# Optimization experiments

Hardware: AMD Instinct MI355X
Metric: run time of the kernel (lower is better)

## Reference

```python
import jax, jax.numpy as jnp
import numpy as np

E = 512
H = 8
D = E // H
WIN = 128  # mask_window_size


def setup_inputs() -> dict:
    key = jax.random.key(0)
    k1, k2, k3, k4, k5 = jax.random.split(key, 5)
    B, L = 2, 4096
    s = 1.0 / np.sqrt(E)
    return {
        "x": jax.random.normal(k1, (B, L, E), dtype=jnp.float32),
        "in_proj_w": jax.random.normal(k2, (3 * E, E), dtype=jnp.float32) * s,
        "in_proj_b": jax.random.normal(k3, (3 * E,), dtype=jnp.float32) * 0.02,
        "out_w": jax.random.normal(k4, (E, E), dtype=jnp.float32) * s,
        "out_b": jax.random.normal(k5, (E,), dtype=jnp.float32) * 0.02,
    }


def reference(x, in_proj_w, in_proj_b, out_w, out_b):
    B, L, _ = x.shape
    # fused qkv projection (torch MultiheadAttention in_proj): x @ W.T + b
    qkv = jnp.einsum("ble,fe->blf", x, in_proj_w) + in_proj_b  # [B,L,3E]
    q, k, v = jnp.split(qkv, 3, axis=-1)
    # [B,H,L,D]
    q = q.reshape(B, L, H, D).transpose(0, 2, 1, 3)
    k = k.reshape(B, L, H, D).transpose(0, 2, 1, 3)
    v = v.reshape(B, L, H, D).transpose(0, 2, 1, 3)
    scores = jnp.einsum("bhqd,bhkd->bhqk", q, k) / jnp.sqrt(jnp.float32(D))
    # (diagonal stays blocked — faithful to the original gen_mask quirk)
    idx = jnp.arange(L)
    dist = jnp.abs(idx[:, None] - idx[None, :])
    blocked = (dist > WIN) | (dist == 0)  # [L,L]
    scores = jnp.where(blocked[None, None], -jnp.inf, scores)
    attn = jax.nn.softmax(scores, axis=-1)  # [B,H,L,L]
    out = jnp.einsum("bhqk,bhkd->bhqd", attn, v)  # [B,H,L,D]
    out = out.transpose(0, 2, 1, 3).reshape(B, L, E)
    return jnp.einsum("ble,fe->blf", out, out_w) + out_b
```

## Files before the change

### kernel.cpp

```cpp
#include <hip/hip_runtime.h>
#include <math.h>

#define E_DIM 512
#define H_DIM 8
#define WIN 128
#define L_SEQ 4096
#define B_SZ 2

typedef unsigned short ushort_t;
typedef unsigned int uint_t;
typedef __attribute__((ext_vector_type(8))) __bf16 bf16x8;
typedef __attribute__((ext_vector_type(4))) float f32x4;

__device__ __forceinline__ ushort_t f2bf(float f) {
    uint_t u = __float_as_uint(f);
    u = u + 0x7fffu + ((u >> 16) & 1u);
    return (ushort_t)(u >> 16);
}
__device__ __forceinline__ float bf2f(ushort_t h) {
    return __uint_as_float((uint_t)h << 16);
}

__device__ __forceinline__ void gload16(const ushort_t* g, ushort_t* l) {
    __builtin_amdgcn_global_load_lds(
        (const __attribute__((address_space(1))) void*)g,
        (__attribute__((address_space(3))) void*)l,
        16, 0, 0);
}


__global__ __launch_bounds__(256) void convertX(
    const float* __restrict__ x,  ushort_t* __restrict__ xh,
    const float* __restrict__ w1, ushort_t* __restrict__ w1h,
    const float* __restrict__ w2, ushort_t* __restrict__ w2h) {
    int sg = blockIdx.x * 256 + threadIdx.x;
    const float* src; ushort_t* dh;
    if (sg < 524288)      { src = x;  dh = xh; }
    else if (sg < 622592) { src = w1; dh = w1h; sg -= 524288; }
    else                  { src = w2; dh = w2h; sg -= 622592; }
    const int tile = sg >> 6, slot = sg & 63;
    const int row = (tile >> 4) * 16 + (slot & 15);
    const int k   = (tile & 15) * 32 + (slot >> 4) * 8;
    const float4 v0 = *(const float4*)&src[(size_t)row * 512 + k];
    const float4 v1 = *(const float4*)&src[(size_t)row * 512 + k + 4];
    const float vv[8] = {v0.x, v0.y, v0.z, v0.w, v1.x, v1.y, v1.z, v1.w};
    union { ushort_t u[8]; ushort4 v[2]; } h;
    #pragma unroll
    for (int j = 0; j < 8; j++) h.u[j] = f2bf(vv[j]);
    ((ushort4*)(dh + (size_t)sg * 8))[0] = h.v[0];
    ((ushort4*)(dh + (size_t)sg * 8))[1] = h.v[1];
}

__global__ __launch_bounds__(256) void gemm_qkv(
    const ushort_t* __restrict__ Ah,
    const ushort_t* __restrict__ Wh,
    const float* __restrict__ bias,
    ushort_t* __restrict__ qTh, ushort_t* __restrict__ qTl,
    ushort_t* __restrict__ kTh, ushort_t* __restrict__ kTl,
    ushort_t* __restrict__ vTh) {
    __shared__ __align__(16) ushort_t sAh[2][8 * 512];
    __shared__ __align__(16) ushort_t sWh[2][8 * 512];

    const int tid = threadIdx.x, lane = tid & 63, w = tid >> 6;
    const int wm = w & 1, wn = w >> 1, ln = lane & 15, quad = lane >> 4;
    const int bx = blockIdx.x, by = blockIdx.y;
    const int lo8 = lane * 8;
    const int wu = __builtin_amdgcn_readfirstlane(w);

    f32x4 acc[4][4];
    const f32x4 zero = {0.f, 0.f, 0.f, 0.f};
    #pragma unroll
    for (int i = 0; i < 4; i++)
        #pragma unroll
        for (int j = 0; j < 4; j++) acc[i][j] = zero;

    const ushort_t* pb[4];
    ushort_t* db0[4];
    ushort_t* db1[4];
    #pragma unroll
    for (int t = 0; t < 4; t++) {
        const int g = wu * 4 + t;
        if (g < 8) {
            pb[t] = Ah + ((size_t)(bx * 8 + g) * 16) * 512;
            db0[t] = &sAh[0][g * 512]; db1[t] = &sAh[1][g * 512];
        } else {
            const int u = g - 8;
            pb[t] = Wh + ((size_t)(by * 8 + u) * 16) * 512;
            db0[t] = &sWh[0][u * 512]; db1[t] = &sWh[1][u * 512];
        }
    }

    #pragma unroll
    for (int t = 0; t < 4; t++)
        gload16(pb[t] + lo8, db0[t]);

    for (int kt = 0; kt < 16; kt++) {
        __syncthreads();
        if (kt < 15) {
            const int koff = (kt + 1) * 512;
            if ((kt + 1) & 1) {
                #pragma unroll
                for (int t = 0; t < 4; t++) gload16(pb[t] + koff + lo8, db1[t]);
            } else {
                #pragma unroll
                for (int t = 0; t < 4; t++) gload16(pb[t] + koff + lo8, db0[t]);
            }
        }
        const int cb = kt & 1;
        bf16x8 fah[4];
        #pragma unroll
        for (int i = 0; i < 4; i++)
            fah[i] = *(const bf16x8*)&sAh[cb][(wm * 4 + i) * 512 + lo8];
        #pragma unroll
        for (int j = 0; j < 4; j++) {
            const bf16x8 fbh = *(const bf16x8*)&sWh[cb][(wn * 4 + j) * 512 + lo8];
            #pragma unroll
            for (int i = 0; i < 4; i++)
                acc[i][j] = __builtin_amdgcn_mfma_f32_16x16x32_bf16(fah[i], fbh, acc[i][j], 0, 0, 0);
        }
    }

    const int b = bx >> 5;
    const int h = 2 * (by & 3) + wn;
    if (by < 8) {
        ushort_t* dh = (by < 4) ? qTh : kTh;
        ushort_t* dl = (by < 4) ? qTl : kTl;
        #pragma unroll
        for (int i = 0; i < 4; i++) {
            const int rt = (bx & 31) * 8 + wm * 4 + i;
            const size_t tb = ((size_t)(b * 8 + h) * 256 + rt) * 2;
            #pragma unroll
            for (int j = 0; j < 4; j++) {
                const float bv = bias[by * 128 + wn * 64 + j * 16 + ln];
                const size_t tile = tb + (j >> 1);
                #pragma unroll
                for (int r = 0; r < 4; r++) {
                    const int slot = ((j * 2 + (ln >> 3)) & 3) * 16 + quad * 4 + r;
                    const size_t idx = tile * 512 + slot * 8 + (ln & 7);
                    const float v = acc[i][j][r] + bv;
                    const ushort_t hh = f2bf(v);
                    dh[idx] = hh;
                    dl[idx] = f2bf(v - bf2f(hh));
                }
            }
        }
    } else {
        const int kwin = (bx & 31) * 2 + wm;
        #pragma unroll
        for (int i = 0; i < 4; i++) {
            const int kk = i >> 1;
            #pragma unroll
            for (int j = 0; j < 4; j++) {
                const float bv = bias[by * 128 + wn * 64 + j * 16 + ln];
                const size_t tile = (((size_t)(b * 8 + h) * 64 + kwin) * 4 + j) * 2 + kk;
                #pragma unroll
                for (int r = 0; r < 4; r++) {
                    const int klq = quad * 4 + r;
                    const int slot = ((i & 1) * 2 + (klq >> 3)) * 16 + ln;
                    const size_t idx = tile * 512 + slot * 8 + (klq & 7);
                    vTh[idx] = f2bf(acc[i][j][r] + bv);
                }
            }
        }
    }
}

__global__ __launch_bounds__(512) void attn_mfma(
    const ushort_t* __restrict__ qTh, const ushort_t* __restrict__ qTl,
    const ushort_t* __restrict__ kTh, const ushort_t* __restrict__ kTl,
    const ushort_t* __restrict__ vTh,
    ushort_t* __restrict__ outh) {
    __shared__ __align__(16) ushort_t sKh[8 * 512];
    __shared__ __align__(16) ushort_t sKl[8 * 512];
    __shared__ __align__(16) ushort_t sV [8 * 512];
    __shared__ __align__(16) ushort_t sP [16 * 512];

    const int qs = blockIdx.x * 128;
    const int h = blockIdx.y, b = blockIdx.z;
    const int bh = b * 8 + h;
    const int tid = threadIdx.x, lane = tid & 63;
    const int w = tid >> 6, ln = lane & 15, quad = lane >> 4;
    const int lo8 = lane * 8;

    bf16x8 qf[2][2];
    {
        const size_t qt = ((size_t)bh * 256 + (qs >> 4) + w) * 2;
        qf[0][0] = *(const bf16x8*)(qTh + (qt + 0) * 512 + lo8);
        qf[1][0] = *(const bf16x8*)(qTh + (qt + 1) * 512 + lo8);
        qf[0][1] = *(const bf16x8*)(qTl + (qt + 0) * 512 + lo8);
        qf[1][1] = *(const bf16x8*)(qTl + (qt + 1) * 512 + lo8);
    }

    f32x4 oacc[4];
    const f32x4 zero = {0.f, 0.f, 0.f, 0.f};
    #pragma unroll
    for (int dt = 0; dt < 4; dt++) oacc[dt] = zero;
    float m_run[4], l_run[4];
    #pragma unroll
    for (int r = 0; r < 4; r++) { m_run[r] = -1e30f; l_run[r] = 0.f; }

    const float cscale = 0.125f * 1.44269504f;
    const int qlo = qs + 16 * w;

    for (int kt = 0; kt < 6; kt++) {
        const int ks = qs - 128 + kt * 64;

        __syncthreads();

        if (w < 4) {
            int st = (qs >> 4) - 8 + kt * 4 + w;
            st = st < 0 ? 0 : (st > 255 ? 255 : st);
            const size_t kb = ((size_t)bh * 256 + st) * 2 * 512 + lo8;
            gload16(kTh + kb,       &sKh[(w * 2 + 0) * 512]);
            gload16(kTh + kb + 512, &sKh[(w * 2 + 1) * 512]);
            gload16(kTl + kb,       &sKl[(w * 2 + 0) * 512]);
            gload16(kTl + kb + 512, &sKl[(w * 2 + 1) * 512]);
        } else {
            const int u = w - 4;
            int vw = (qs >> 6) - 2 + kt;
            vw = vw < 0 ? 0 : (vw > 63 ? 63 : vw);
            const size_t vb = (((size_t)bh * 64 + vw) * 4 + u) * 2 * 512 + lo8;
            gload16(vTh + vb,       &sV[(u * 2 + 0) * 512]);
            gload16(vTh + vb + 512, &sV[(u * 2 + 1) * 512]);
        }
        __syncthreads();

        f32x4 sacc[4];
        #pragma unroll
        for (int jt = 0; jt < 4; jt++) {
            f32x4 a = zero;
            const int klo = ks + 16 * jt;
            const bool dead = (klo > qlo + 15 + WIN) || (klo + 15 < qlo - WIN) ||
                              (klo >= L_SEQ) || (klo + 15 < 0);
            if (!dead) {
                #pragma unroll
                for (int kk = 0; kk < 2; kk++) {
                    const bf16x8 kh = *(const bf16x8*)&sKh[(jt * 2 + kk) * 512 + lo8];
                    const bf16x8 klo2 = *(const bf16x8*)&sKl[(jt * 2 + kk) * 512 + lo8];
                    a = __builtin_amdgcn_mfma_f32_16x16x32_bf16(qf[kk][0], kh, a, 0, 0, 0);
                    a = __builtin_amdgcn_mfma_f32_16x16x32_bf16(qf[kk][0], klo2, a, 0, 0, 0);
                    a = __builtin_amdgcn_mfma_f32_16x16x32_bf16(qf[kk][1], kh, a, 0, 0, 0);
                }
            }
            sacc[jt] = a;
        }

        float u[4][4];
        #pragma unroll
        for (int jt = 0; jt < 4; jt++) {
            const int kcol = ks + 16 * jt + ln;
            #pragma unroll
            for (int r = 0; r < 4; r++) {
                const int qrow = qlo + quad * 4 + r;
                const int dist = qrow > kcol ? qrow - kcol : kcol - qrow;
                const bool ok = (kcol >= 0) && (kcol < L_SEQ) && (dist >= 1) && (dist <= WIN);
                u[jt][r] = ok ? sacc[jt][r] * cscale : -INFINITY;
            }
        }
        float mk[4];
        #pragma unroll
        for (int r = 0; r < 4; r++)
            mk[r] = fmaxf(fmaxf(u[0][r], u[1][r]), fmaxf(u[2][r], u[3][r]));
        #pragma unroll
        for (int off = 1; off <= 8; off <<= 1)
            #pragma unroll
            for (int r = 0; r < 4; r++)
                mk[r] = fmaxf(mk[r], __shfl_xor(mk[r], off));

        float alpha[4], psum[4], p[4][4];
        #pragma unroll
        for (int r = 0; r < 4; r++) {
            const float mnew = fmaxf(fmaxf(m_run[r], mk[r]), -1e30f);
            alpha[r] = exp2f(m_run[r] - mnew);
            m_run[r] = mnew;
            psum[r] = 0.f;
            #pragma unroll
            for (int jt = 0; jt < 4; jt++) {
                p[jt][r] = exp2f(u[jt][r] - mnew);
                psum[r] += p[jt][r];
            }
        }
        #pragma unroll
        for (int off = 1; off <= 8; off <<= 1)
            #pragma unroll
            for (int r = 0; r < 4; r++)
                psum[r] += __shfl_xor(psum[r], off);
        #pragma unroll
        for (int r = 0; r < 4; r++)
            l_run[r] = l_run[r] * alpha[r] + psum[r];

        #pragma unroll
        for (int dt = 0; dt < 4; dt++)
            #pragma unroll
            for (int r = 0; r < 4; r++)
                oacc[dt][r] *= alpha[r];

        #pragma unroll
        for (int jt = 0; jt < 4; jt++)
            #pragma unroll
            for (int r = 0; r < 4; r++) {
                const int slot = ((jt & 1) * 2 + (ln >> 3)) * 16 + quad * 4 + r;
                sP[w * 1024 + (jt >> 1) * 512 + slot * 8 + (ln & 7)] = f2bf(p[jt][r]);
            }

        #pragma unroll
        for (int kk = 0; kk < 2; kk++) {
            const bf16x8 pf = *(const bf16x8*)&sP[w * 1024 + kk * 512 + lo8];
            #pragma unroll
            for (int dt = 0; dt < 4; dt++) {
                const bf16x8 vf = *(const bf16x8*)&sV[(dt * 2 + kk) * 512 + lo8];
                oacc[dt] = __builtin_amdgcn_mfma_f32_16x16x32_bf16(pf, vf, oacc[dt], 0, 0, 0);
            }
        }
    }

    const int Rt = ((b * L_SEQ + qs) >> 4) + w;
    #pragma unroll
    for (int r = 0; r < 4; r++) {
        const float inv_l = 1.f / l_run[r];
        #pragma unroll
        for (int dt = 0; dt < 4; dt++) {
            const float v = oacc[dt][r] * inv_l;
            const int tile = Rt * 16 + h * 2 + (dt >> 1);
            const int slot = ((dt & 1) * 2 + (ln >> 3)) * 16 + quad * 4 + r;
            const size_t idx = (size_t)tile * 512 + slot * 8 + (ln & 7);
            outh[idx] = f2bf(v);
        }
    }
}

__global__ __launch_bounds__(512) void gemm_out(
    const ushort_t* __restrict__ Ah,
    const ushort_t* __restrict__ Wh,
    const float* __restrict__ bias, float* __restrict__ C) {
    __shared__ __align__(16) ushort_t sAh[2][16 * 512];
    __shared__ __align__(16) ushort_t sWh[2][8 * 512];

    const int tid = threadIdx.x, lane = tid & 63, w = tid >> 6;
    const int wm = w & 3, wn = w >> 2, ln = lane & 15, quad = lane >> 4;
    const int bx = blockIdx.x, by = blockIdx.y;
    const int lo8 = lane * 8;
    const int wu = __builtin_amdgcn_readfirstlane(w);

    f32x4 acc[2][2];
    const f32x4 zero = {0.f, 0.f, 0.f, 0.f};
    #pragma unroll
    for (int i = 0; i < 2; i++)
        #pragma unroll
        for (int j = 0; j < 2; j++) acc[i][j] = zero;

    const ushort_t* pb[3];
    ushort_t* db0[3];
    ushort_t* db1[3];
    #pragma unroll
    for (int t = 0; t < 3; t++) {
        const int g = wu * 3 + t;
        if (g < 16) {
            pb[t] = Ah + ((size_t)(bx * 8 + (g >> 1)) * 16 + (g & 1)) * 512;
            db0[t] = &sAh[0][g * 512]; db1[t] = &sAh[1][g * 512];
        } else {
            const int u = g - 16;
            pb[t] = Wh + ((size_t)(by * 4 + (u >> 1)) * 16 + (u & 1)) * 512;
            db0[t] = &sWh[0][u * 512]; db1[t] = &sWh[1][u * 512];
        }
    }

    #pragma unroll
    for (int t = 0; t < 3; t++)
        gload16(pb[t] + lo8, db0[t]);

    for (int KT = 0; KT < 8; KT++) {
        __syncthreads();
        if (KT < 7) {
            const int koff = (KT + 1) * 1024;
            if ((KT + 1) & 1) {
                #pragma unroll
                for (int t = 0; t < 3; t++) gload16(pb[t] + koff + lo8, db1[t]);
            } else {
                #pragma unroll
                for (int t = 0; t < 3; t++) gload16(pb[t] + koff + lo8, db0[t]);
            }
        }
        const int cb = KT & 1;
        #pragma unroll
        for (int ks = 0; ks < 2; ks++) {
            bf16x8 fah[2];
            #pragma unroll
            for (int i = 0; i < 2; i++)
                fah[i] = *(const bf16x8*)&sAh[cb][((wm * 2 + i) * 2 + ks) * 512 + lo8];
            #pragma unroll
            for (int j = 0; j < 2; j++) {
                const bf16x8 fbh = *(const bf16x8*)&sWh[cb][((wn * 2 + j) * 2 + ks) * 512 + lo8];
                #pragma unroll
                for (int i = 0; i < 2; i++)
                    acc[i][j] = __builtin_amdgcn_mfma_f32_16x16x32_bf16(fah[i], fbh, acc[i][j], 0, 0, 0);
            }
        }
    }

    #pragma unroll
    for (int i = 0; i < 2; i++) {
        const int row0 = bx * 128 + wm * 32 + i * 16 + quad * 4;
        #pragma unroll
        for (int j = 0; j < 2; j++) {
            const int col = by * 64 + wn * 32 + j * 16 + ln;
            const float bv = bias[col];
            #pragma unroll
            for (int r = 0; r < 4; r++)
                C[(size_t)(row0 + r) * E_DIM + col] = acc[i][j][r] + bv;
        }
    }
}

extern "C" void kernel_launch(void* const* d_in, const int* in_sizes, int n_in,
                              void* d_out, int out_size, void* d_ws, size_t ws_size,
                              hipStream_t stream) {
    const float* x         = (const float*)d_in[0];
    const float* in_proj_w = (const float*)d_in[1];
    const float* in_proj_b = (const float*)d_in[2];
    const float* out_w     = (const float*)d_in[3];
    const float* out_b     = (const float*)d_in[4];
    float* out = (float*)d_out;

    const int N = B_SZ * L_SEQ;
    const size_t NE = (size_t)N * E_DIM;

    char* p = (char*)d_ws;
    ushort_t* xh  = (ushort_t*)p; p += NE * 2;
    ushort_t* w1h = (ushort_t*)p; p += (size_t)3 * E_DIM * E_DIM * 2;
    ushort_t* w2h = (ushort_t*)p; p += (size_t)E_DIM * E_DIM * 2;
    ushort_t* qTh = (ushort_t*)p; p += NE * 2;
    ushort_t* qTl = (ushort_t*)p; p += NE * 2;
    ushort_t* kTh = (ushort_t*)p; p += NE * 2;
    ushort_t* kTl = (ushort_t*)p; p += NE * 2;
    ushort_t* vTh = (ushort_t*)p; p += NE * 2;
    ushort_t* ath = (ushort_t*)p; p += NE * 2;

    convertX<<<2560, 256, 0, stream>>>(x, xh, in_proj_w, w1h, out_w, w2h);

    gemm_qkv<<<dim3(64, 12), 256, 0, stream>>>(
        xh, w1h, in_proj_b, qTh, qTl, kTh, kTl, vTh);

    attn_mfma<<<dim3(L_SEQ / 128, H_DIM, B_SZ), 512, 0, stream>>>(
        qTh, qTl, kTh, kTl, vTh, ath);

    gemm_out<<<dim3(64, 8), 512, 0, stream>>>(
        ath, w2h, out_b, out);
}
```

Baseline: 144.3 us.

## Drop bf16 hi/lo split for Q and K and double-buffer K/V tiles

Q and K are now stored as a single bf16 copy instead of a high/low pair. This halves QKV-projection stores and attention loads, and cuts the QK^T MFMAs from three per step to one. The freed shared memory double-buffers the K and V tiles, so the next tile's loads are issued before the current tile's compute and the second barrier per iteration is gone. In exchange, attention scores lose the extra precision the split gave, so accuracy may drift against an fp32 reference.

```diff
diff --git a/kernel.cpp b/kernel.cpp
--- a/kernel.cpp
+++ b/kernel.cpp
@@ -55,8 +55,8 @@
     const ushort_t* __restrict__ Ah,
     const ushort_t* __restrict__ Wh,
     const float* __restrict__ bias,
-    ushort_t* __restrict__ qTh, ushort_t* __restrict__ qTl,
-    ushort_t* __restrict__ kTh, ushort_t* __restrict__ kTl,
+    ushort_t* __restrict__ qTh,
+    ushort_t* __restrict__ kTh,
     ushort_t* __restrict__ vTh) {
     __shared__ __align__(16) ushort_t sAh[2][8 * 512];
     __shared__ __align__(16) ushort_t sWh[2][8 * 512];
@@ -124,7 +124,6 @@
     const int h = 2 * (by & 3) + wn;
     if (by < 8) {
         ushort_t* dh = (by < 4) ? qTh : kTh;
-        ushort_t* dl = (by < 4) ? qTl : kTl;
         #pragma unroll
         for (int i = 0; i < 4; i++) {
             const int rt = (bx & 31) * 8 + wm * 4 + i;
@@ -137,10 +136,7 @@
                 for (int r = 0; r < 4; r++) {
                     const int slot = ((j * 2 + (ln >> 3)) & 3) * 16 + quad * 4 + r;
                     const size_t idx = tile * 512 + slot * 8 + (ln & 7);
-                    const float v = acc[i][j][r] + bv;
-                    const ushort_t hh = f2bf(v);
-                    dh[idx] = hh;
-                    dl[idx] = f2bf(v - bf2f(hh));
+                    dh[idx] = f2bf(acc[i][j][r] + bv);
                 }
             }
         }
@@ -166,13 +162,12 @@
 }
 
 __global__ __launch_bounds__(512) void attn_mfma(
-    const ushort_t* __restrict__ qTh, const ushort_t* __restrict__ qTl,
-    const ushort_t* __restrict__ kTh, const ushort_t* __restrict__ kTl,
+    const ushort_t* __restrict__ qTh,
+    const ushort_t* __restrict__ kTh,
     const ushort_t* __restrict__ vTh,
     ushort_t* __restrict__ outh) {
-    __shared__ __align__(16) ushort_t sKh[8 * 512];
-    __shared__ __align__(16) ushort_t sKl[8 * 512];
-    __shared__ __align__(16) ushort_t sV [8 * 512];
+    __shared__ __align__(16) ushort_t sKh[2][8 * 512];
+    __shared__ __align__(16) ushort_t sV [2][8 * 512];
     __shared__ __align__(16) ushort_t sP [16 * 512];
 
     const int qs = blockIdx.x * 128;
@@ -182,13 +177,11 @@
     const int w = tid >> 6, ln = lane & 15, quad = lane >> 4;
     const int lo8 = lane * 8;
 
-    bf16x8 qf[2][2];
+    bf16x8 qf[2];
     {
         const size_t qt = ((size_t)bh * 256 + (qs >> 4) + w) * 2;
-        qf[0][0] = *(const bf16x8*)(qTh + (qt + 0) * 512 + lo8);
-        qf[1][0] = *(const bf16x8*)(qTh + (qt + 1) * 512 + lo8);
-        qf[0][1] = *(const bf16x8*)(qTl + (qt + 0) * 512 + lo8);
-        qf[1][1] = *(const bf16x8*)(qTl + (qt + 1) * 512 + lo8);
+        qf[0] = *(const bf16x8*)(qTh + (qt + 0) * 512 + lo8);
+        qf[1] = *(const bf16x8*)(qTh + (qt + 1) * 512 + lo8);
     }
 
     f32x4 oacc[4];
@@ -202,28 +195,46 @@
     const float cscale = 0.125f * 1.44269504f;
     const int qlo = qs + 16 * w;
 
+    {
+        if (w < 4) {
+            int st = (qs >> 4) - 8 + w;
+            st = st < 0 ? 0 : (st > 255 ? 255 : st);
+            const size_t kb = ((size_t)bh * 256 + st) * 2 * 512 + lo8;
+            gload16(kTh + kb,       &sKh[0][(w * 2 + 0) * 512]);
+            gload16(kTh + kb + 512, &sKh[0][(w * 2 + 1) * 512]);
+        } else {
+            const int u = w - 4;
+            int vw = (qs >> 6) - 2;
+            vw = vw < 0 ? 0 : (vw > 63 ? 63 : vw);
+            const size_t vb = (((size_t)bh * 64 + vw) * 4 + u) * 2 * 512 + lo8;
+            gload16(vTh + vb,       &sV[0][(u * 2 + 0) * 512]);
+            gload16(vTh + vb + 512, &sV[0][(u * 2 + 1) * 512]);
+        }
+    }
+
     for (int kt = 0; kt < 6; kt++) {
         const int ks = qs - 128 + kt * 64;
 
         __syncthreads();
 
-        if (w < 4) {
-            int st = (qs >> 4) - 8 + kt * 4 + w;
-            st = st < 0 ? 0 : (st > 255 ? 255 : st);
-            const size_t kb = ((size_t)bh * 256 + st) * 2 * 512 + lo8;
-            gload16(kTh + kb,       &sKh[(w * 2 + 0) * 512]);
-            gload16(kTh + kb + 512, &sKh[(w * 2 + 1) * 512]);
-            gload16(kTl + kb,       &sKl[(w * 2 + 0) * 512]);
-            gload16(kTl + kb + 512, &sKl[(w * 2 + 1) * 512]);
-        } else {
-            const int u = w - 4;
-            int vw = (qs >> 6) - 2 + kt;
-            vw = vw < 0 ? 0 : (vw > 63 ? 63 : vw);
-            const size_t vb = (((size_t)bh * 64 + vw) * 4 + u) * 2 * 512 + lo8;
-            gload16(vTh + vb,       &sV[(u * 2 + 0) * 512]);
-            gload16(vTh + vb + 512, &sV[(u * 2 + 1) * 512]);
-        }
-        __syncthreads();
+        if (kt < 5) {
+            const int nb = (kt + 1) & 1;
+            if (w < 4) {
+                int st = (qs >> 4) - 8 + (kt + 1) * 4 + w;
+                st = st < 0 ? 0 : (st > 255 ? 255 : st);
+                const size_t kb = ((size_t)bh * 256 + st) * 2 * 512 + lo8;
+                gload16(kTh + kb,       &sKh[nb][(w * 2 + 0) * 512]);
+                gload16(kTh + kb + 512, &sKh[nb][(w * 2 + 1) * 512]);
+            } else {
+                const int u = w - 4;
+                int vw = (qs >> 6) - 2 + kt + 1;
+                vw = vw < 0 ? 0 : (vw > 63 ? 63 : vw);
+                const size_t vb = (((size_t)bh * 64 + vw) * 4 + u) * 2 * 512 + lo8;
+                gload16(vTh + vb,       &sV[nb][(u * 2 + 0) * 512]);
+                gload16(vTh + vb + 512, &sV[nb][(u * 2 + 1) * 512]);
+            }
+        }
+        const int cb = kt & 1;
 
         f32x4 sacc[4];
         #pragma unroll
@@ -235,11 +246,8 @@
             if (!dead) {
                 #pragma unroll
                 for (int kk = 0; kk < 2; kk++) {
-                    const bf16x8 kh = *(const bf16x8*)&sKh[(jt * 2 + kk) * 512 + lo8];
-                    const bf16x8 klo2 = *(const bf16x8*)&sKl[(jt * 2 + kk) * 512 + lo8];
-                    a = __builtin_amdgcn_mfma_f32_16x16x32_bf16(qf[kk][0], kh, a, 0, 0, 0);
-                    a = __builtin_amdgcn_mfma_f32_16x16x32_bf16(qf[kk][0], klo2, a, 0, 0, 0);
-                    a = __builtin_amdgcn_mfma_f32_16x16x32_bf16(qf[kk][1], kh, a, 0, 0, 0);
+                    const bf16x8 kh = *(const bf16x8*)&sKh[cb][(jt * 2 + kk) * 512 + lo8];
+                    a = __builtin_amdgcn_mfma_f32_16x16x32_bf16(qf[kk], kh, a, 0, 0, 0);
                 }
             }
             sacc[jt] = a;
@@ -308,7 +316,7 @@
             const bf16x8 pf = *(const bf16x8*)&sP[w * 1024 + kk * 512 + lo8];
             #pragma unroll
             for (int dt = 0; dt < 4; dt++) {
-                const bf16x8 vf = *(const bf16x8*)&sV[(dt * 2 + kk) * 512 + lo8];
+                const bf16x8 vf = *(const bf16x8*)&sV[cb][(dt * 2 + kk) * 512 + lo8];
                 oacc[dt] = __builtin_amdgcn_mfma_f32_16x16x32_bf16(pf, vf, oacc[dt], 0, 0, 0);
             }
         }
@@ -430,19 +438,17 @@
     ushort_t* w1h = (ushort_t*)p; p += (size_t)3 * E_DIM * E_DIM * 2;
     ushort_t* w2h = (ushort_t*)p; p += (size_t)E_DIM * E_DIM * 2;
     ushort_t* qTh = (ushort_t*)p; p += NE * 2;
-    ushort_t* qTl = (ushort_t*)p; p += NE * 2;
     ushort_t* kTh = (ushort_t*)p; p += NE * 2;
-    ushort_t* kTl = (ushort_t*)p; p += NE * 2;
     ushort_t* vTh = (ushort_t*)p; p += NE * 2;
     ushort_t* ath = (ushort_t*)p; p += NE * 2;
 
     convertX<<<2560, 256, 0, stream>>>(x, xh, in_proj_w, w1h, out_w, w2h);
 
     gemm_qkv<<<dim3(64, 12), 256, 0, stream>>>(
-        xh, w1h, in_proj_b, qTh, qTl, kTh, kTl, vTh);
+        xh, w1h, in_proj_b, qTh, kTh, vTh);
 
     attn_mfma<<<dim3(L_SEQ / 128, H_DIM, B_SZ), 512, 0, stream>>>(
-        qTh, qTl, kTh, kTl, vTh, ath);
+        qTh, kTh, vTh, ath);
 
     gemm_out<<<dim3(64, 8), 512, 0, stream>>>(
         ath, w2h, out_b, out);
```

Result: faster. 135.0 us, median of 2 (-6.5%).
